# Kernel optimization log

Measured on AMD Instinct MI355X. Metric: run time of the kernel, lower is better.

The kernel has to match this reference:

```python
import jax, jax.numpy as jnp
import numpy as np

N = 100000
E = 1600000
BN_EPS = 1e-3  # Keras BatchNormalization default epsilon


def setup_inputs() -> dict:
    key = jax.random.key(0)
    ks = jax.random.split(key, 24)
    inp = {
        'x': jax.random.normal(ks[0], (N, 128), jnp.float32),
        'edge_src': jax.random.randint(ks[1], (E,), 0, N, jnp.int32),
        'edge_dst': jnp.sort(jax.random.randint(ks[2], (E,), 0, N, jnp.int32)),
        'edge_w': jax.random.uniform(ks[3], (E,), jnp.float32),
        'bn1_gamma': jnp.ones((128,), jnp.float32),
        'bn1_beta': jnp.zeros((128,), jnp.float32),
        'bn1_mean': jax.random.normal(ks[4], (128,), jnp.float32),
        'bn1_var': jax.random.uniform(ks[5], (128,), jnp.float32),
        'gat_w': jax.random.normal(ks[6], (128, 128), jnp.float32) * 0.09,
        'gat_a_self': jax.random.normal(ks[7], (128,), jnp.float32) * 0.09,
        'gat_a_nbr': jax.random.normal(ks[8], (128,), jnp.float32) * 0.09,
        'gat_b': jnp.zeros((128,), jnp.float32),
        'bn2_gamma': jnp.ones((128,), jnp.float32),
        'bn2_beta': jnp.zeros((128,), jnp.float32),
        'bn2_mean': jax.random.normal(ks[9], (128,), jnp.float32),
        'bn2_var': jax.random.uniform(ks[10], (128,), jnp.float32),
        'gcn2_w': jax.random.normal(ks[11], (128, 64), jnp.float32) * 0.09,
        'gcn2_b': jnp.zeros((64,), jnp.float32),
        'bn3_gamma': jnp.ones((64,), jnp.float32),
        'bn3_beta': jnp.zeros((64,), jnp.float32),
        'bn3_mean': jax.random.normal(ks[12], (64,), jnp.float32),
        'bn3_var': jax.random.uniform(ks[13], (64,), jnp.float32),
        'gcn3_w': jax.random.normal(ks[14], (64, 32), jnp.float32) * 0.12,
        'gcn3_b': jnp.zeros((32,), jnp.float32),
        'zm_w': jax.random.normal(ks[15], (32, 64), jnp.float32) * 0.18,
        'zm_b': jnp.zeros((64,), jnp.float32),
        'zv_w': jax.random.normal(ks[16], (32, 64), jnp.float32) * 0.18,
        'zv_b': jnp.zeros((64,), jnp.float32),
        'eps': jax.random.normal(ks[17], (N, 64), jnp.float32),
    }
    return inp


def _bn(x, gamma, beta, mean, var):
    # Keras BatchNormalization, inference mode (moving statistics).
    return gamma * (x - mean) * jax.lax.rsqrt(var + BN_EPS) + beta


def _gat(x, edge_src, edge_dst, w, a_self, a_nbr, b, n):
    h = x @ w                                   # [N, C]
    att_i = h @ a_self                          # [N] target score
    att_j = h @ a_nbr                           # [N] source score
    e = jax.nn.leaky_relu(att_i[edge_dst] + att_j[edge_src], 0.2)  # [E]
    m = jax.ops.segment_max(e, edge_dst, num_segments=n)
    p = jnp.exp(e - m[edge_dst])
    s = jax.ops.segment_sum(p, edge_dst, num_segments=n)
    alpha = p / s[edge_dst]                     # segment softmax over in-edges
    out = jax.ops.segment_sum(alpha[:, None] * h[edge_src], edge_dst, num_segments=n)
    return jax.nn.relu(out + b)


def _gcn(x, edge_src, edge_dst, edge_w, w, b, n):
    h = x @ w                                   # [N, C]
    out = jax.ops.segment_sum(edge_w[:, None] * h[edge_src], edge_dst, num_segments=n)
    return jax.nn.relu(out + b)


def reference(x, edge_src, edge_dst, edge_w,
              bn1_gamma, bn1_beta, bn1_mean, bn1_var,
              gat_w, gat_a_self, gat_a_nbr, gat_b,
              bn2_gamma, bn2_beta, bn2_mean, bn2_var,
              gcn2_w, gcn2_b,
              bn3_gamma, bn3_beta, bn3_mean, bn3_var,
              gcn3_w, gcn3_b,
              zm_w, zm_b, zv_w, zv_b, eps):
    n = x.shape[0]
    h = _bn(x, bn1_gamma, bn1_beta, bn1_mean, bn1_var)
    h = _gat(h, edge_src, edge_dst, gat_w, gat_a_self, gat_a_nbr, gat_b, n)
    # dropout layers are identity at inference
    h = _bn(h, bn2_gamma, bn2_beta, bn2_mean, bn2_var)
    h = _gcn(h, edge_src, edge_dst, edge_w, gcn2_w, gcn2_b, n)
    h = _bn(h, bn3_gamma, bn3_beta, bn3_mean, bn3_var)
    h = _gcn(h, edge_src, edge_dst, edge_w, gcn3_w, gcn3_b, n)
    # Flatten on [N, F] is identity
    z_mean = jax.nn.sigmoid(h @ zm_w + zm_b)
    z_log_var = h @ zv_w + zv_b
    z = z_mean + jnp.exp(0.5 * z_log_var) * eps
    return (z_mean, z_log_var, z)
```

## Files before the change

### kernel.cpp

```cpp
#include <hip/hip_runtime.h>
#include <math.h>


#define BN_EPS 1e-3f

typedef __attribute__((ext_vector_type(8))) short bf16x8;
typedef __attribute__((ext_vector_type(4))) float f32x4;

__device__ __forceinline__ unsigned bf2(float lo, float hi) {
  unsigned ul = __float_as_uint(lo), uh = __float_as_uint(hi);
  ul = (ul + 0x7FFFu + ((ul >> 16) & 1u)) >> 16;
  uh = (uh + 0x7FFFu + ((uh >> 16) & 1u)) >> 16;
  return ul | (uh << 16);
}
__device__ __forceinline__ unsigned short bf1(float x) {
  unsigned u = __float_as_uint(x);
  return (unsigned short)((u + 0x7FFFu + ((u >> 16) & 1u)) >> 16);
}
__device__ __forceinline__ float4 ub4(uint2 p) {
  float4 r;
  r.x = __uint_as_float(p.x << 16);
  r.y = __uint_as_float(p.x & 0xFFFF0000u);
  r.z = __uint_as_float(p.y << 16);
  r.w = __uint_as_float(p.y & 0xFFFF0000u);
  return r;
}

__global__ __launch_bounds__(256) void prep_rowptr_kernel(
    const float* __restrict__ bn1g, const float* __restrict__ bn1b,
    const float* __restrict__ bn1m, const float* __restrict__ bn1v,
    const float* __restrict__ gatw,
    const float* __restrict__ bn2g, const float* __restrict__ bn2b,
    const float* __restrict__ bn2m, const float* __restrict__ bn2v,
    const float* __restrict__ gcn2w,
    const float* __restrict__ bn3g, const float* __restrict__ bn3b,
    const float* __restrict__ bn3m, const float* __restrict__ bn3v,
    const float* __restrict__ gcn3w,
    unsigned short* __restrict__ Wt1b, float* __restrict__ bW1,
    unsigned short* __restrict__ Wt2b, float* __restrict__ bW2,
    unsigned short* __restrict__ Wt3b, float* __restrict__ bW3,
    const int* __restrict__ dst, int* __restrict__ rp, int n, int e) {
  const int t = threadIdx.x;
  if (blockIdx.x != 0) {
    int i = (blockIdx.x - 1) * 256 + t;
    if (i > n) return;
    int lo = 0, hi = e;
    while (lo < hi) {
      int mid = (lo + hi) >> 1;
      if (dst[mid] < i) lo = mid + 1; else hi = mid;
    }
    rp[i] = lo;
    return;
  }
  __shared__ float a1[128], b1[128], a2[128], b2[128], a3[64], b3[64];
  if (t < 128) {
    float a = bn1g[t] * (1.0f / sqrtf(bn1v[t] + BN_EPS));
    a1[t] = a; b1[t] = bn1b[t] - bn1m[t] * a;
    float c = bn2g[t] * (1.0f / sqrtf(bn2v[t] + BN_EPS));
    a2[t] = c; b2[t] = bn2b[t] - bn2m[t] * c;
    if (t < 64) {
      float d = bn3g[t] * (1.0f / sqrtf(bn3v[t] + BN_EPS));
      a3[t] = d; b3[t] = bn3b[t] - bn3m[t] * d;
    }
  }
  __syncthreads();
  for (int idx = t; idx < 128 * 128; idx += 256) {
    int c = idx >> 7, k = idx & 127;
    Wt1b[idx] = bf1(a1[k] * gatw[k * 128 + c]);
  }
  for (int idx = t; idx < 64 * 128; idx += 256) {
    int c = idx >> 7, k = idx & 127;
    Wt2b[idx] = bf1(a2[k] * gcn2w[k * 64 + c]);
  }
  for (int idx = t; idx < 32 * 64; idx += 256) {
    int c = idx >> 6, k = idx & 63;
    Wt3b[idx] = bf1(a3[k] * gcn3w[k * 32 + c]);
  }
  if (t < 128) { float s = 0.f; for (int k = 0; k < 128; k++) s += b1[k] * gatw[k * 128 + t]; bW1[t] = s; }
  if (t < 64)  { float s = 0.f; for (int k = 0; k < 128; k++) s += b2[k] * gcn2w[k * 64 + t]; bW2[t] = s; }
  if (t < 32)  { float s = 0.f; for (int k = 0; k < 64; k++)  s += b3[k] * gcn3w[k * 32 + t]; bW3[t] = s; }
}

template <int K, int C, bool DO_ATT, bool IN_BF16>
__global__ __launch_bounds__(256) void gemm_mfma(
    const void* __restrict__ in, const unsigned short* __restrict__ Wtb,
    const float* __restrict__ bW, unsigned short* __restrict__ outb, int n,
    const float* __restrict__ aself, const float* __restrict__ anbr,
    float* __restrict__ atti, float* __restrict__ attj) {
  constexpr int KCH = K / 32;
  constexpr int MB = C / 16;
  const int wid = (blockIdx.x << 2) + (threadIdx.x >> 6);
  const int lane = threadIdx.x & 63;
  const int node0 = wid * 16;
  if (node0 >= n) return;
  const int ln = lane & 15;
  const int kg = lane >> 4;
  const int nd = node0 + ln;
  const int ndc = (nd < n) ? nd : (n - 1);
  bf16x8 bfr[KCH];
  if constexpr (IN_BF16) {
    const bf16x8* __restrict__ inr =
        (const bf16x8*)((const unsigned short*)in + (size_t)ndc * K);
#pragma unroll
    for (int kc = 0; kc < KCH; kc++) bfr[kc] = inr[kc * 4 + kg];
  } else {
    const float4* __restrict__ inr =
        (const float4*)((const float*)in + (size_t)ndc * K);
#pragma unroll
    for (int kc = 0; kc < KCH; kc++) {
      float4 u0 = inr[kc * 8 + kg * 2];
      float4 u1 = inr[kc * 8 + kg * 2 + 1];
      union { uint4 u; bf16x8 v; } pk;
      pk.u.x = bf2(u0.x, u0.y); pk.u.y = bf2(u0.z, u0.w);
      pk.u.z = bf2(u1.x, u1.y); pk.u.w = bf2(u1.z, u1.w);
      bfr[kc] = pk.v;
    }
  }
  float sa = 0.f, sj = 0.f;
#pragma unroll
  for (int m = 0; m < MB; m++) {
    f32x4 acc = {0.f, 0.f, 0.f, 0.f};
#pragma unroll
    for (int kc = 0; kc < KCH; kc++) {
      bf16x8 af = *(const bf16x8*)&Wtb[(size_t)(m * 16 + ln) * K + kc * 32 + kg * 8];
      acc = __builtin_amdgcn_mfma_f32_16x16x32_bf16(af, bfr[kc], acc, 0, 0, 0);
    }
    const int c0 = m * 16 + kg * 4;
    float4 bv = *(const float4*)&bW[c0];
    float o0 = acc[0] + bv.x, o1 = acc[1] + bv.y;
    float o2 = acc[2] + bv.z, o3 = acc[3] + bv.w;
    if (nd < n) {
      uint2 p; p.x = bf2(o0, o1); p.y = bf2(o2, o3);
      *(uint2*)&outb[(size_t)nd * C + c0] = p;
    }
    if constexpr (DO_ATT) {
      float4 as = *(const float4*)&aself[c0];
      float4 an = *(const float4*)&anbr[c0];
      sa += o0 * as.x + o1 * as.y + o2 * as.z + o3 * as.w;
      sj += o0 * an.x + o1 * an.y + o2 * an.z + o3 * an.w;
    }
  }
  if constexpr (DO_ATT) {
    sa += __shfl_xor(sa, 16); sa += __shfl_xor(sa, 32);
    sj += __shfl_xor(sj, 16); sj += __shfl_xor(sj, 32);
    if (kg == 0 && nd < n) { atti[nd] = sa; attj[nd] = sj; }
  }
}

__global__ __launch_bounds__(256) void gat_kernel(
    const unsigned short* __restrict__ h1b, const float* __restrict__ att_i,
    const float* __restrict__ att_j, const int* __restrict__ src,
    const int* __restrict__ rp, const float* __restrict__ bias,
    unsigned short* __restrict__ outb, int n) {
  const int node = (blockIdx.x * 256 + threadIdx.x) >> 6;
  const int lane = threadIdx.x & 63;
  if (node >= n) return;
  const int cg = lane & 31;
  const int eg = lane >> 5;
  const int start = rp[node];
  const int deg = rp[node + 1] - start;
  if (deg == 0) {
    if (eg == 0) {
      float4 b = ((const float4*)bias)[cg];
      uint2 p;
      p.x = bf2(fmaxf(b.x, 0.f), fmaxf(b.y, 0.f));
      p.y = bf2(fmaxf(b.z, 0.f), fmaxf(b.w, 0.f));
      ((uint2*)outb)[(unsigned)node * 32 + cg] = p;
    }
    return;
  }
  const uint2* __restrict__ h2v = (const uint2*)h1b;
  const float ai = att_i[node];
  float4 av[4];
#pragma unroll
  for (int k = 0; k < 4; k++) av[k] = {0.f, 0.f, 0.f, 0.f};
  float ss = 0.f, m_run = -INFINITY;
  for (int chunk = 0; chunk < deg; chunk += 64) {
    const int cnt = min(64, deg - chunk);
    int sv = 0; float v = -INFINITY;
    if (lane < cnt) {
      sv = src[start + chunk + lane];
      float a = ai + att_j[sv];
      v = (a >= 0.f) ? a : 0.2f * a;
    }
    float m = v;
#pragma unroll
    for (int off = 32; off; off >>= 1) m = fmaxf(m, __shfl_xor(m, off));
    const float m_new = fmaxf(m_run, m);
    const float scale = __expf(m_run - m_new);
#pragma unroll
    for (int k = 0; k < 4; k++) {
      av[k].x *= scale; av[k].y *= scale; av[k].z *= scale; av[k].w *= scale;
    }
    const float p = (lane < cnt) ? __expf(v - m_new) : 0.f;
    float ps = p;
#pragma unroll
    for (int off = 32; off; off >>= 1) ps += __shfl_xor(ps, off);
    ss = ss * scale + ps;
    m_run = m_new;
    for (int j2 = 0; j2 < cnt; j2 += 16) {
      float pk[8]; int sk[8];
#pragma unroll
      for (int k = 0; k < 8; k++) {
        int j = j2 + 2 * k + eg;
        pk[k] = __shfl(p, j);
        sk[k] = __shfl(sv, j);
      }
      uint2 hk[8];
#pragma unroll
      for (int k = 0; k < 8; k++) hk[k] = h2v[(unsigned)sk[k] * 32 + cg];
#pragma unroll
      for (int k = 0; k < 8; k++) {
        float4 hv = ub4(hk[k]);
        av[k & 3].x = fmaf(pk[k], hv.x, av[k & 3].x);
        av[k & 3].y = fmaf(pk[k], hv.y, av[k & 3].y);
        av[k & 3].z = fmaf(pk[k], hv.z, av[k & 3].z);
        av[k & 3].w = fmaf(pk[k], hv.w, av[k & 3].w);
      }
    }
  }
  float4 a0;
  a0.x = av[0].x + av[1].x + av[2].x + av[3].x;
  a0.y = av[0].y + av[1].y + av[2].y + av[3].y;
  a0.z = av[0].z + av[1].z + av[2].z + av[3].z;
  a0.w = av[0].w + av[1].w + av[2].w + av[3].w;
  a0.x += __shfl_xor(a0.x, 32); a0.y += __shfl_xor(a0.y, 32);
  a0.z += __shfl_xor(a0.z, 32); a0.w += __shfl_xor(a0.w, 32);
  if (eg == 0) {
    const float inv = 1.0f / ss;
    float4 b = ((const float4*)bias)[cg];
    float o0 = fmaxf(fmaf(a0.x, inv, b.x), 0.f);
    float o1 = fmaxf(fmaf(a0.y, inv, b.y), 0.f);
    float o2 = fmaxf(fmaf(a0.z, inv, b.z), 0.f);
    float o3 = fmaxf(fmaf(a0.w, inv, b.w), 0.f);
    uint2 p; p.x = bf2(o0, o1); p.y = bf2(o2, o3);
    ((uint2*)outb)[(unsigned)node * 32 + cg] = p;
  }
}

template <int C, int NCH>
__global__ __launch_bounds__(256) void gcn_agg_kernel(
    const unsigned short* __restrict__ hb, const int* __restrict__ src,
    const float* __restrict__ ew, const int* __restrict__ rp,
    const float* __restrict__ bias, unsigned short* __restrict__ outb, int n) {
  constexpr int CG = C / 4;
  constexpr int EGN = 64 / CG;
  const int node = (blockIdx.x * 256 + threadIdx.x) >> 6;
  const int lane = threadIdx.x & 63;
  if (node >= n) return;
  const int cg = lane % CG;
  const int eg = lane / CG;
  const int start = rp[node];
  const int deg = rp[node + 1] - start;
  const uint2* __restrict__ h2v = (const uint2*)hb;
  float4 av[4];
#pragma unroll
  for (int k = 0; k < 4; k++) av[k] = {0.f, 0.f, 0.f, 0.f};
  for (int chunk = 0; chunk < deg; chunk += 64) {
    const int cnt = min(64, deg - chunk);
    int sv = 0; float wv = 0.f;
    if (lane < cnt) {
      sv = src[start + chunk + lane];
      wv = ew[start + chunk + lane];
    }
    for (int j2 = 0; j2 < cnt; j2 += NCH * EGN) {
      float wk[NCH]; int sk[NCH];
#pragma unroll
      for (int k = 0; k < NCH; k++) {
        int j = j2 + k * EGN + eg;
        wk[k] = __shfl(wv, j);
        sk[k] = __shfl(sv, j);
      }
      uint2 hk[NCH];
#pragma unroll
      for (int k = 0; k < NCH; k++) hk[k] = h2v[(unsigned)sk[k] * CG + cg];
#pragma unroll
      for (int k = 0; k < NCH; k++) {
        float4 hv = ub4(hk[k]);
        av[k & 3].x = fmaf(wk[k], hv.x, av[k & 3].x);
        av[k & 3].y = fmaf(wk[k], hv.y, av[k & 3].y);
        av[k & 3].z = fmaf(wk[k], hv.z, av[k & 3].z);
        av[k & 3].w = fmaf(wk[k], hv.w, av[k & 3].w);
      }
    }
  }
  float4 a0;
  a0.x = av[0].x + av[1].x + av[2].x + av[3].x;
  a0.y = av[0].y + av[1].y + av[2].y + av[3].y;
  a0.z = av[0].z + av[1].z + av[2].z + av[3].z;
  a0.w = av[0].w + av[1].w + av[2].w + av[3].w;
#pragma unroll
  for (int off = CG; off < 64; off <<= 1) {
    a0.x += __shfl_xor(a0.x, off); a0.y += __shfl_xor(a0.y, off);
    a0.z += __shfl_xor(a0.z, off); a0.w += __shfl_xor(a0.w, off);
  }
  if (eg == 0) {
    float4 b = ((const float4*)bias)[cg];
    float o0 = fmaxf(a0.x + b.x, 0.f);
    float o1 = fmaxf(a0.y + b.y, 0.f);
    float o2 = fmaxf(a0.z + b.z, 0.f);
    float o3 = fmaxf(a0.w + b.w, 0.f);
    uint2 p; p.x = bf2(o0, o1); p.y = bf2(o2, o3);
    ((uint2*)outb)[(unsigned)node * CG + cg] = p;
  }
}

__global__ __launch_bounds__(256) void final_kernel(
    const unsigned short* __restrict__ g3b, const float* __restrict__ zmw,
    const float* __restrict__ zmb, const float* __restrict__ zvw,
    const float* __restrict__ zvb, const float* __restrict__ eps,
    float* __restrict__ out, int n) {
  __shared__ float wm[32 * 64];
  __shared__ float wv[32 * 64];
  __shared__ float xs[4 * 32];
  for (int idx = threadIdx.x; idx < 2048; idx += 256) {
    wm[idx] = zmw[idx];
    wv[idx] = zvw[idx];
  }
  const float bm = zmb[threadIdx.x & 63];
  const float bv = zvb[threadIdx.x & 63];
  const size_t n64 = (size_t)n * 64;
  for (int pass = 0; pass < 16; pass++) {
    const int nb = blockIdx.x * 64 + pass * 4;
    __syncthreads();
    if (threadIdx.x < 128) {
      size_t idx = (size_t)nb * 32 + threadIdx.x;
      float vv = 0.f;
      if (idx < (size_t)n * 32)
        vv = __uint_as_float((unsigned)g3b[idx] << 16);
      xs[threadIdx.x] = vv;
    }
    __syncthreads();
    const int node = nb + (threadIdx.x >> 6);
    if (node >= n) continue;
    const int c = threadIdx.x & 63;
    const float* x = &xs[(threadIdx.x >> 6) * 32];
    float am = 0.f, avv = 0.f;
#pragma unroll
    for (int k = 0; k < 32; k++) {
      float xv = x[k];
      am = fmaf(xv, wm[k * 64 + c], am);
      avv = fmaf(xv, wv[k * 64 + c], avv);
    }
    am += bm;
    avv += bv;
    float zm = 1.f / (1.f + __expf(-am));
    float ex = __expf(fminf(0.5f * avv, 85.0f));
    float z = fmaf(ex, eps[(size_t)node * 64 + c], zm);
    size_t o = (size_t)node * 64 + c;
    out[o] = zm;
    out[n64 + o] = avv;
    out[2 * n64 + o] = z;
  }
}

extern "C" void kernel_launch(void* const* d_in, const int* in_sizes, int n_in,
                              void* d_out, int out_size, void* d_ws, size_t ws_size,
                              hipStream_t stream) {
  const float* x     = (const float*)d_in[0];
  const int*   esrc  = (const int*)d_in[1];
  const int*   edst  = (const int*)d_in[2];
  const float* ew    = (const float*)d_in[3];
  const float* bn1g  = (const float*)d_in[4];
  const float* bn1b  = (const float*)d_in[5];
  const float* bn1m  = (const float*)d_in[6];
  const float* bn1v  = (const float*)d_in[7];
  const float* gatw  = (const float*)d_in[8];
  const float* aself = (const float*)d_in[9];
  const float* anbr  = (const float*)d_in[10];
  const float* gatb  = (const float*)d_in[11];
  const float* bn2g  = (const float*)d_in[12];
  const float* bn2b  = (const float*)d_in[13];
  const float* bn2m  = (const float*)d_in[14];
  const float* bn2v  = (const float*)d_in[15];
  const float* gcn2w = (const float*)d_in[16];
  const float* gcn2b = (const float*)d_in[17];
  const float* bn3g  = (const float*)d_in[18];
  const float* bn3b  = (const float*)d_in[19];
  const float* bn3m  = (const float*)d_in[20];
  const float* bn3v  = (const float*)d_in[21];
  const float* gcn3w = (const float*)d_in[22];
  const float* gcn3b = (const float*)d_in[23];
  const float* zmw   = (const float*)d_in[24];
  const float* zmb   = (const float*)d_in[25];
  const float* zvw   = (const float*)d_in[26];
  const float* zvb   = (const float*)d_in[27];
  const float* eps   = (const float*)d_in[28];
  float* out = (float*)d_out;

  const int n = in_sizes[0] / 128;
  const int E = in_sizes[1];

  char* base = (char*)d_ws;
  size_t off = 0;
  auto alloc = [&](size_t bytes) -> char* {
    char* p = base + off;
    off += (bytes + 255) & ~(size_t)255;
    return p;
  };
  int*   rp   = (int*)alloc((size_t)(n + 1) * 4);
  unsigned short* Wt1b = (unsigned short*)alloc(128 * 128 * 2);
  float* bW1  = (float*)alloc(128 * 4);
  unsigned short* Wt2b = (unsigned short*)alloc(64 * 128 * 2);
  float* bW2  = (float*)alloc(64 * 4);
  unsigned short* Wt3b = (unsigned short*)alloc(32 * 64 * 2);
  float* bW3  = (float*)alloc(32 * 4);
  float* atti = (float*)alloc((size_t)n * 4);
  float* attj = (float*)alloc((size_t)n * 4);
  unsigned short* h1b = (unsigned short*)alloc((size_t)n * 128 * 2);
  unsigned short* g1b = (unsigned short*)alloc((size_t)n * 128 * 2);
  unsigned short* h2b = (unsigned short*)alloc((size_t)n * 64 * 2);
  unsigned short* g2b = h1b;
  unsigned short* h3b = g1b;
  unsigned short* g3b = h2b;

  const int rpb = (n + 1 + 255) / 256;
  prep_rowptr_kernel<<<rpb + 1, 256, 0, stream>>>(
      bn1g, bn1b, bn1m, bn1v, gatw, bn2g, bn2b, bn2m, bn2v, gcn2w,
      bn3g, bn3b, bn3m, bn3v, gcn3w,
      Wt1b, bW1, Wt2b, bW2, Wt3b, bW3, edst, rp, n, E);

  const int gw = (n + 15) / 16;
  const int gb = (gw + 3) / 4;

  gemm_mfma<128, 128, true, false><<<gb, 256, 0, stream>>>(
      x, Wt1b, bW1, h1b, n, aself, anbr, atti, attj);
  gat_kernel<<<(n + 3) / 4, 256, 0, stream>>>(
      h1b, atti, attj, esrc, rp, gatb, g1b, n);

  gemm_mfma<128, 64, false, true><<<gb, 256, 0, stream>>>(
      g1b, Wt2b, bW2, h2b, n, nullptr, nullptr, nullptr, nullptr);
  gcn_agg_kernel<64, 8><<<(n + 3) / 4, 256, 0, stream>>>(
      h2b, esrc, ew, rp, gcn2b, g2b, n);

  gemm_mfma<64, 32, false, true><<<gb, 256, 0, stream>>>(
      g2b, Wt3b, bW3, h3b, n, nullptr, nullptr, nullptr, nullptr);
  gcn_agg_kernel<32, 4><<<(n + 3) / 4, 256, 0, stream>>>(
      h3b, esrc, ew, rp, gcn3b, g3b, n);

  final_kernel<<<(n + 63) / 64, 256, 0, stream>>>(
      g3b, zmw, zmb, zvw, zvb, eps, out, n);
}
```

Baseline: 452.8 us.

## Map one node per half-wave in GAT and use packed FMA for aggregation

The GAT aggregation kernel now assigns one node to each 32-lane half-wavefront instead of a full 64-lane wave. It processes edges in chunks of 32, skips the softmax rescale on the first chunk, and removes the cross-half reduction, so the launch uses twice as many nodes per block. Both the GAT and GCN aggregation loops switch to inline-asm v_pk_fma_f32 packed FMAs on bf16-unpacked pairs, halving FMA instruction count. The tradeoff is fewer edges in flight per node and less latency hiding for the gathers when nodes have high degree.

After: 438.5 us. 3.1% less time.

```diff
diff --git a/kernel.cpp b/kernel.cpp
--- a/kernel.cpp
+++ b/kernel.cpp
@@ -6,6 +6,13 @@
 
 typedef __attribute__((ext_vector_type(8))) short bf16x8;
 typedef __attribute__((ext_vector_type(4))) float f32x4;
+typedef __attribute__((ext_vector_type(2))) float f32x2;
+
+__device__ __forceinline__ f32x2 pkfma(f32x2 a, f32x2 b, f32x2 c) {
+  f32x2 d;
+  asm("v_pk_fma_f32 %0, %1, %2, %3" : "=v"(d) : "v"(a), "v"(b), "v"(c));
+  return d;
+}
 
 __device__ __forceinline__ unsigned bf2(float lo, float hi) {
   unsigned ul = __float_as_uint(lo), uh = __float_as_uint(hi);
@@ -17,12 +24,10 @@
   unsigned u = __float_as_uint(x);
   return (unsigned short)((u + 0x7FFFu + ((u >> 16) & 1u)) >> 16);
 }
-__device__ __forceinline__ float4 ub4(uint2 p) {
-  float4 r;
-  r.x = __uint_as_float(p.x << 16);
-  r.y = __uint_as_float(p.x & 0xFFFF0000u);
-  r.z = __uint_as_float(p.y << 16);
-  r.w = __uint_as_float(p.y & 0xFFFF0000u);
+__device__ __forceinline__ f32x2 ub2(unsigned u) {
+  f32x2 r;
+  r.x = __uint_as_float(u << 16);
+  r.y = __uint_as_float(u & 0xFFFF0000u);
   return r;
 }
 
@@ -152,90 +157,82 @@
     const float* __restrict__ att_j, const int* __restrict__ src,
     const int* __restrict__ rp, const float* __restrict__ bias,
     unsigned short* __restrict__ outb, int n) {
-  const int node = (blockIdx.x * 256 + threadIdx.x) >> 6;
-  const int lane = threadIdx.x & 63;
+  const int node = (blockIdx.x * 256 + threadIdx.x) >> 5;
+  const int sl = threadIdx.x & 31;
+  const int gbase = threadIdx.x & 32;
   if (node >= n) return;
-  const int cg = lane & 31;
-  const int eg = lane >> 5;
   const int start = rp[node];
   const int deg = rp[node + 1] - start;
   if (deg == 0) {
-    if (eg == 0) {
-      float4 b = ((const float4*)bias)[cg];
-      uint2 p;
-      p.x = bf2(fmaxf(b.x, 0.f), fmaxf(b.y, 0.f));
-      p.y = bf2(fmaxf(b.z, 0.f), fmaxf(b.w, 0.f));
-      ((uint2*)outb)[(unsigned)node * 32 + cg] = p;
-    }
+    float4 b = ((const float4*)bias)[sl];
+    uint2 p;
+    p.x = bf2(fmaxf(b.x, 0.f), fmaxf(b.y, 0.f));
+    p.y = bf2(fmaxf(b.z, 0.f), fmaxf(b.w, 0.f));
+    ((uint2*)outb)[(unsigned)node * 32 + sl] = p;
     return;
   }
   const uint2* __restrict__ h2v = (const uint2*)h1b;
   const float ai = att_i[node];
-  float4 av[4];
-#pragma unroll
-  for (int k = 0; k < 4; k++) av[k] = {0.f, 0.f, 0.f, 0.f};
+  f32x2 av[8];
+#pragma unroll
+  for (int k = 0; k < 8; k++) av[k] = {0.f, 0.f};
   float ss = 0.f, m_run = -INFINITY;
-  for (int chunk = 0; chunk < deg; chunk += 64) {
-    const int cnt = min(64, deg - chunk);
+  for (int chunk = 0; chunk < deg; chunk += 32) {
+    const int cnt = min(32, deg - chunk);
     int sv = 0; float v = -INFINITY;
-    if (lane < cnt) {
-      sv = src[start + chunk + lane];
+    if (sl < cnt) {
+      sv = src[start + chunk + sl];
       float a = ai + att_j[sv];
       v = (a >= 0.f) ? a : 0.2f * a;
     }
     float m = v;
 #pragma unroll
-    for (int off = 32; off; off >>= 1) m = fmaxf(m, __shfl_xor(m, off));
+    for (int off = 16; off; off >>= 1) m = fmaxf(m, __shfl_xor(m, off));
     const float m_new = fmaxf(m_run, m);
-    const float scale = __expf(m_run - m_new);
-#pragma unroll
-    for (int k = 0; k < 4; k++) {
-      av[k].x *= scale; av[k].y *= scale; av[k].z *= scale; av[k].w *= scale;
-    }
-    const float p = (lane < cnt) ? __expf(v - m_new) : 0.f;
+    if (chunk) {
+      const float scale = __expf(m_run - m_new);
+#pragma unroll
+      for (int k = 0; k < 8; k++) { av[k].x *= scale; av[k].y *= scale; }
+      ss *= scale;
+    }
+    const float p = (sl < cnt) ? __expf(v - m_new) : 0.f;
     float ps = p;
 #pragma unroll
-    for (int off = 32; off; off >>= 1) ps += __shfl_xor(ps, off);
-    ss = ss * scale + ps;
+    for (int off = 16; off; off >>= 1) ps += __shfl_xor(ps, off);
+    ss += ps;
     m_run = m_new;
-    for (int j2 = 0; j2 < cnt; j2 += 16) {
+    for (int j2 = 0; j2 < cnt; j2 += 8) {
       float pk[8]; int sk[8];
 #pragma unroll
       for (int k = 0; k < 8; k++) {
-        int j = j2 + 2 * k + eg;
+        int j = gbase + j2 + k;
         pk[k] = __shfl(p, j);
         sk[k] = __shfl(sv, j);
       }
       uint2 hk[8];
 #pragma unroll
-      for (int k = 0; k < 8; k++) hk[k] = h2v[(unsigned)sk[k] * 32 + cg];
+      for (int k = 0; k < 8; k++) hk[k] = h2v[(unsigned)sk[k] * 32 + sl];
 #pragma unroll
       for (int k = 0; k < 8; k++) {
-        float4 hv = ub4(hk[k]);
-        av[k & 3].x = fmaf(pk[k], hv.x, av[k & 3].x);
-        av[k & 3].y = fmaf(pk[k], hv.y, av[k & 3].y);
-        av[k & 3].z = fmaf(pk[k], hv.z, av[k & 3].z);
-        av[k & 3].w = fmaf(pk[k], hv.w, av[k & 3].w);
+        f32x2 pd = {pk[k], pk[k]};
+        av[(k & 3) * 2]     = pkfma(ub2(hk[k].x), pd, av[(k & 3) * 2]);
+        av[(k & 3) * 2 + 1] = pkfma(ub2(hk[k].y), pd, av[(k & 3) * 2 + 1]);
       }
     }
   }
-  float4 a0;
-  a0.x = av[0].x + av[1].x + av[2].x + av[3].x;
-  a0.y = av[0].y + av[1].y + av[2].y + av[3].y;
-  a0.z = av[0].z + av[1].z + av[2].z + av[3].z;
-  a0.w = av[0].w + av[1].w + av[2].w + av[3].w;
-  a0.x += __shfl_xor(a0.x, 32); a0.y += __shfl_xor(a0.y, 32);
-  a0.z += __shfl_xor(a0.z, 32); a0.w += __shfl_xor(a0.w, 32);
-  if (eg == 0) {
-    const float inv = 1.0f / ss;
-    float4 b = ((const float4*)bias)[cg];
-    float o0 = fmaxf(fmaf(a0.x, inv, b.x), 0.f);
-    float o1 = fmaxf(fmaf(a0.y, inv, b.y), 0.f);
-    float o2 = fmaxf(fmaf(a0.z, inv, b.z), 0.f);
-    float o3 = fmaxf(fmaf(a0.w, inv, b.w), 0.f);
-    uint2 p; p.x = bf2(o0, o1); p.y = bf2(o2, o3);
-    ((uint2*)outb)[(unsigned)node * 32 + cg] = p;
-  }
+  f32x2 s0, s1;
+  s0.x = av[0].x + av[2].x + av[4].x + av[6].x;
+  s0.y = av[0].y + av[2].y + av[4].y + av[6].y;
+  s1.x = av[1].x + av[3].x + av[5].x + av[7].x;
+  s1.y = av[1].y + av[3].y + av[5].y + av[7].y;
+  const float inv = 1.0f / ss;
+  float4 b = ((const float4*)bias)[sl];
+  float o0 = fmaxf(fmaf(s0.x, inv, b.x), 0.f);
+  float o1 = fmaxf(fmaf(s0.y, inv, b.y), 0.f);
+  float o2 = fmaxf(fmaf(s1.x, inv, b.z), 0.f);
+  float o3 = fmaxf(fmaf(s1.y, inv, b.w), 0.f);
+  uint2 p; p.x = bf2(o0, o1); p.y = bf2(o2, o3);
+  ((uint2*)outb)[(unsigned)node * 32 + sl] = p;
 }
 
 template <int C, int NCH>
@@ -253,9 +250,9 @@
   const int start = rp[node];
   const int deg = rp[node + 1] - start;
   const uint2* __restrict__ h2v = (const uint2*)hb;
-  float4 av[4];
-#pragma unroll
-  for (int k = 0; k < 4; k++) av[k] = {0.f, 0.f, 0.f, 0.f};
+  f32x2 av[8];
+#pragma unroll
+  for (int k = 0; k < 8; k++) av[k] = {0.f, 0.f};
   for (int chunk = 0; chunk < deg; chunk += 64) {
     const int cnt = min(64, deg - chunk);
     int sv = 0; float wv = 0.f;
@@ -276,30 +273,27 @@
       for (int k = 0; k < NCH; k++) hk[k] = h2v[(unsigned)sk[k] * CG + cg];
 #pragma unroll
       for (int k = 0; k < NCH; k++) {
-        float4 hv = ub4(hk[k]);
-        av[k & 3].x = fmaf(wk[k], hv.x, av[k & 3].x);
-        av[k & 3].y = fmaf(wk[k], hv.y, av[k & 3].y);
-        av[k & 3].z = fmaf(wk[k], hv.z, av[k & 3].z);
-        av[k & 3].w = fmaf(wk[k], hv.w, av[k & 3].w);
+        f32x2 wd = {wk[k], wk[k]};
+        av[(k & 3) * 2]     = pkfma(ub2(hk[k].x), wd, av[(k & 3) * 2]);
+        av[(k & 3) * 2 + 1] = pkfma(ub2(hk[k].y), wd, av[(k & 3) * 2 + 1]);
       }
     }
   }
-  float4 a0;
-  a0.x = av[0].x + av[1].x + av[2].x + av[3].x;
-  a0.y = av[0].y + av[1].y + av[2].y + av[3].y;
-  a0.z = av[0].z + av[1].z + av[2].z + av[3].z;
-  a0.w = av[0].w + av[1].w + av[2].w + av[3].w;
+  float a0 = av[0].x + av[2].x + av[4].x + av[6].x;
+  float a1 = av[0].y + av[2].y + av[4].y + av[6].y;
+  float a2 = av[1].x + av[3].x + av[5].x + av[7].x;
+  float a3 = av[1].y + av[3].y + av[5].y + av[7].y;
 #pragma unroll
   for (int off = CG; off < 64; off <<= 1) {
-    a0.x += __shfl_xor(a0.x, off); a0.y += __shfl_xor(a0.y, off);
-    a0.z += __shfl_xor(a0.z, off); a0.w += __shfl_xor(a0.w, off);
+    a0 += __shfl_xor(a0, off); a1 += __shfl_xor(a1, off);
+    a2 += __shfl_xor(a2, off); a3 += __shfl_xor(a3, off);
   }
   if (eg == 0) {
     float4 b = ((const float4*)bias)[cg];
-    float o0 = fmaxf(a0.x + b.x, 0.f);
-    float o1 = fmaxf(a0.y + b.y, 0.f);
-    float o2 = fmaxf(a0.z + b.z, 0.f);
-    float o3 = fmaxf(a0.w + b.w, 0.f);
+    float o0 = fmaxf(a0 + b.x, 0.f);
+    float o1 = fmaxf(a1 + b.y, 0.f);
+    float o2 = fmaxf(a2 + b.z, 0.f);
+    float o3 = fmaxf(a3 + b.w, 0.f);
     uint2 p; p.x = bf2(o0, o1); p.y = bf2(o2, o3);
     ((uint2*)outb)[(unsigned)node * CG + cg] = p;
   }
@@ -425,7 +419,7 @@
 
   gemm_mfma<128, 128, true, false><<<gb, 256, 0, stream>>>(
       x, Wt1b, bW1, h1b, n, aself, anbr, atti, attj);
-  gat_kernel<<<(n + 3) / 4, 256, 0, stream>>>(
+  gat_kernel<<<(n + 7) / 8, 256, 0, stream>>>(
       h1b, atti, attj, esrc, rp, gatb, g1b, n);
 
   gemm_mfma<128, 64, false, true><<<gb, 256, 0, stream>>>(
```
